# Kernel tuning notes

Hardware: AMD Instinct MI355X
Metric: run time of the kernel (lower is better)

## Reference

```python
import jax, jax.numpy as jnp
import numpy as np
from jax import lax

DIM, D_INNER, D_STATE, D_CONV, DT_RANK = 256, 512, 16, 4, 16
B_, H_, W_ = 4, 64, 64


def setup_inputs() -> dict:
    key = jax.random.key(0)
    ks = jax.random.split(key, 10)
    s = lambda k, shape, scale: (jax.random.normal(k, shape, dtype=jnp.float32) * scale)
    inp = {
        "x": s(ks[0], (B_, DIM, H_, W_), 1.0),
        "in_proj_w": s(ks[1], (2 * D_INNER, DIM), DIM ** -0.5),
        "conv_w": s(ks[2], (D_INNER, 1, D_CONV), D_CONV ** -0.5),
        "conv_b": s(ks[3], (D_INNER,), 0.02),
        "x_proj_w": s(ks[4], (DT_RANK + 2 * D_STATE, D_INNER), D_INNER ** -0.5),
        "dt_proj_w": s(ks[5], (D_INNER, DT_RANK), DT_RANK ** -0.5),
        "dt_proj_b": s(ks[6], (D_INNER,), 0.02),
        # A_log init: log(arange(1..d_state)) broadcast over channels (standard S4D-real init)
        "A_log": jnp.broadcast_to(jnp.log(jnp.arange(1, D_STATE + 1, dtype=jnp.float32)), (D_INNER, D_STATE)).copy(),
        "D": jnp.ones((D_INNER,), dtype=jnp.float32),
        "out_proj_w": s(ks[7], (DIM, D_INNER), D_INNER ** -0.5),
    }
    return inp


def _mamba_forward(x, in_proj_w, conv_w, conv_b, x_proj_w, dt_proj_w, dt_proj_b, A_log, D, out_proj_w):
    b, c, h, w = x.shape
    L = h * w
    xs = x.reshape(b, c, L).transpose(0, 2, 1)                      # [b, L, dim]

    xz = jnp.einsum('bld,ed->ble', xs, in_proj_w)                   # [b, L, 2*d_inner]
    u, res = jnp.split(xz, 2, axis=-1)                              # each [b, L, d_inner]

    # causal depthwise conv1d over sequence
    u_t = u.transpose(0, 2, 1)                                      # [b, d_inner, L]
    u_t = lax.conv_general_dilated(u_t, conv_w, window_strides=(1,),
                                   padding=[(D_CONV - 1, 0)],
                                   feature_group_count=D_INNER,
                                   dimension_numbers=('NCH', 'OIH', 'NCH'))
    u = jax.nn.silu(u_t.transpose(0, 2, 1) + conv_b)                # [b, L, d_inner]

    dbc = jnp.einsum('bld,ed->ble', u, x_proj_w)                    # [b, L, dt_rank+2n]
    dt, Bm, Cm = jnp.split(dbc, [DT_RANK, DT_RANK + D_STATE], axis=-1)
    delta = jax.nn.softplus(jnp.einsum('blr,dr->bld', dt, dt_proj_w) + dt_proj_b)  # [b,L,d_inner]

    A = -jnp.exp(A_log)                                             # [d_inner, n]
    deltaA = jnp.exp(jnp.einsum('bld,dn->bldn', delta, A))          # [b,L,d,n]
    deltaBu = jnp.einsum('bld,bln,bld->bldn', delta, Bm, u)         # [b,L,d,n]

    def step(state, inp):
        dA, dBu, c_t = inp                                          # [b,d,n],[b,d,n],[b,n]
        state = dA * state + dBu
        y = jnp.einsum('bdn,bn->bd', state, c_t)
        return state, y

    init = jnp.zeros((b, D_INNER, D_STATE), dtype=x.dtype)
    _, ys = lax.scan(step, init, (jnp.moveaxis(deltaA, 1, 0),
                                  jnp.moveaxis(deltaBu, 1, 0),
                                  jnp.moveaxis(Cm, 1, 0)))
    y = jnp.moveaxis(ys, 0, 1) + u * D                              # [b, L, d_inner]
    y = y * jax.nn.silu(res)
    out = jnp.einsum('ble,de->bld', y, out_proj_w)                  # [b, L, dim]
    return out.transpose(0, 2, 1).reshape(b, c, h, w)


def reference(x, in_proj_w, conv_w, conv_b, x_proj_w, dt_proj_w, dt_proj_b, A_log, D, out_proj_w):
    return _mamba_forward(x, in_proj_w, conv_w, conv_b, x_proj_w, dt_proj_w, dt_proj_b, A_log, D, out_proj_w)
```

## Files before the change

kernel.cpp:

```cpp
#include <hip/hip_runtime.h>
#include <math.h>


namespace {
constexpr int kB   = 4;
constexpr int kDim = 256;
constexpr int kL   = 4096;
constexpr int kDI  = 512;
constexpr int kN   = 16;
constexpr int kNC  = 128;
constexpr int kCS  = 32;
}

typedef __attribute__((ext_vector_type(8))) short bf16x8;
typedef __attribute__((ext_vector_type(4))) float f32x4;
typedef __attribute__((ext_vector_type(2))) float f32x2;

__device__ __forceinline__ float rcpf(float x) { return __builtin_amdgcn_rcpf(x); }
__device__ __forceinline__ float siluf(float x) { return x * rcpf(1.f + __expf(-x)); }
__device__ __forceinline__ float softplusf(float x) {
  return fmaxf(x, 0.f) + __logf(1.f + __expf(-fabsf(x)));
}

__device__ __forceinline__ unsigned short f2bf(float x) {
  union { float f; unsigned int u; } v; v.f = x;
  unsigned int u = v.u;
  u += 0x7fffu + ((u >> 16) & 1u);
  return (unsigned short)(u >> 16);
}
__device__ __forceinline__ float bf2f(unsigned short u) {
  union { unsigned int i; float f; } v; v.i = ((unsigned int)u) << 16; return v.f;
}

__device__ __forceinline__ void gload_lds16(const void* g, void* l) {
  __builtin_amdgcn_global_load_lds(
      (const __attribute__((address_space(1))) unsigned int*)g,
      (__attribute__((address_space(3))) unsigned int*)l, 16, 0, 0);
}

__global__ __launch_bounds__(256) void k_prep(const float* __restrict__ w_in,
                                              const float* __restrict__ w_out,
                                              const float* __restrict__ w_x,
                                              const float* __restrict__ w_dt,
                                              const float* __restrict__ A_log,
                                              const float* __restrict__ x,
                                              unsigned short* __restrict__ wib,
                                              unsigned short* __restrict__ wob,
                                              unsigned short* __restrict__ wxb,
                                              unsigned short* __restrict__ wdtb,
                                              float* __restrict__ Avz,
                                              unsigned int* __restrict__ flagA,
                                              unsigned short* __restrict__ xt) {
  __shared__ float Xs[64][65];
  const int blk = blockIdx.x;
  const int t = threadIdx.x;
  if (blk < 1760) {
    int idx = blk * 256 + t;
    if (idx < 262144) wib[idx] = f2bf(w_in[idx]);
    else if (idx < 393216) wob[idx - 262144] = f2bf(w_out[idx - 262144]);
    else if (idx < 417792) wxb[idx - 393216] = f2bf(w_x[idx - 393216]);
    else {
      int i = idx - 417792;
      int r = i & 31, d = i >> 5;
      wdtb[i] = (r < 16) ? f2bf(w_dt[d * 16 + r]) : (unsigned short)0;
    }
  } else if (blk < 1762) {
    int d = (blk - 1760) * 256 + t;
    float a0 = -__expf(A_log[d * kN]);
    bool ok = true;
#pragma unroll
    for (int n = 1; n < kN; ++n) {
      float av = -__expf(A_log[d * kN + n]);
      ok = ok && (fabsf(av - (n + 1) * a0) <= 1e-5f * fabsf(av));
    }
    Avz[d] = a0;
    unsigned long long bal = __ballot(ok);
    int wv = t >> 6;
    if ((t & 63) == 0) ((unsigned long long*)Xs)[wv] = bal;
    __syncthreads();
    if (t == 0) {
      unsigned long long all = ~0ull;
#pragma unroll
      for (int w = 0; w < 4; ++w) all &= ((unsigned long long*)Xs)[w];
      flagA[blk - 1760] = (all == ~0ull) ? 1u : 0u;
    }
  } else {
    int id = blk - 1762;
    int lb = id & 63, db = (id >> 6) & 3, b = id >> 8;
    const int d0 = db * 64, l0 = lb * 64, l = t & 63;
#pragma unroll
    for (int rep = 0; rep < 16; ++rep) {
      int dd = rep * 4 + (t >> 6);
      Xs[dd][l] = x[((size_t)b * kDim + d0 + dd) * kL + l0 + l];
    }
    __syncthreads();
#pragma unroll
    for (int rep = 0; rep < 8; ++rep) {
      int lj = rep * 8 + (t >> 5);
      int di = (t & 31) * 2;
      ushort2 v;
      v.x = f2bf(Xs[di][lj]);
      v.y = f2bf(Xs[di + 1][lj]);
      *(ushort2*)(xt + ((size_t)b * kL + l0 + lj) * kDim + d0 + di) = v;
    }
  }
}

__global__ __launch_bounds__(256) void gemm_in_lm(const unsigned short* __restrict__ xt,
                                                  const unsigned short* __restrict__ W,
                                                  unsigned short* __restrict__ ubf,
                                                  unsigned short* __restrict__ resb) {
  __shared__ __align__(16) unsigned short As[128 * 64];
  __shared__ __align__(16) unsigned short Bs[128 * 64];
  const int e0 = blockIdx.x * 128;
  const int l0 = blockIdx.y * 128;
  const int b  = blockIdx.z;
  const int t  = threadIdx.x;
  const int wave = t >> 6, lane = t & 63;
  const int wm = wave >> 1, wn = wave & 1;
  const unsigned short* Ab = xt + (size_t)b * kL * kDim;

  f32x4 acc[4][4];
#pragma unroll
  for (int i = 0; i < 4; ++i)
#pragma unroll
    for (int j = 0; j < 4; ++j) acc[i][j] = (f32x4)0.0f;

  const int srow = t >> 3, sch = t & 7;
  for (int kt = 0; kt < 4; ++kt) {
    const int k0 = kt * 64;
#pragma unroll
    for (int c = 0; c < 4; ++c) {
      int row = c * 32 + srow;
      int gch = sch ^ (row & 7);
      gload_lds16(Ab + (size_t)(l0 + row) * kDim + k0 + gch * 8,
                  (char*)As + c * 4096 + wave * 1024);
      gload_lds16(W  + (size_t)(e0 + row) * kDim + k0 + gch * 8,
                  (char*)Bs + c * 4096 + wave * 1024);
    }
    __syncthreads();
#pragma unroll
    for (int ks = 0; ks < 2; ++ks) {
      bf16x8 af[4], bfr[4];
#pragma unroll
      for (int f = 0; f < 4; ++f) {
        int ra = wm * 64 + f * 16 + (lane & 15);
        int ca = (ks * 4 + (lane >> 4)) ^ (ra & 7);
        af[f] = *(const bf16x8*)((const char*)As + ra * 128 + ca * 16);
        int rb = wn * 64 + f * 16 + (lane & 15);
        int cb = (ks * 4 + (lane >> 4)) ^ (rb & 7);
        bfr[f] = *(const bf16x8*)((const char*)Bs + rb * 128 + cb * 16);
      }
#pragma unroll
      for (int i = 0; i < 4; ++i)
#pragma unroll
        for (int j = 0; j < 4; ++j)
          acc[i][j] = __builtin_amdgcn_mfma_f32_16x16x32_bf16(af[i], bfr[j], acc[i][j], 0, 0, 0);
    }
    __syncthreads();
  }

  const bool is_u = (e0 < kDI);
  unsigned short* dst = is_u ? ubf : resb;
  const int ebase = is_u ? e0 : (e0 - kDI);
#pragma unroll
  for (int i = 0; i < 4; ++i)
#pragma unroll
    for (int j = 0; j < 4; ++j)
#pragma unroll
      for (int r = 0; r < 4; ++r) {
        int l = l0 + wm * 64 + i * 16 + (lane >> 4) * 4 + r;
        int e = ebase + wn * 64 + j * 16 + (lane & 15);
        dst[((size_t)b * kL + l) * kDI + e] = f2bf(acc[i][j][r]);
      }
}

__global__ __launch_bounds__(256) void k_conv(const unsigned short* __restrict__ ubf,
                                              const float* __restrict__ cw,
                                              const float* __restrict__ cb,
                                              unsigned short* __restrict__ ucb) {
  int idx = blockIdx.x * 256 + threadIdx.x;
  int d8 = idx & 63;
  int l  = (idx >> 6) & (kL - 1);
  int b  = idx >> 18;
  int d0 = d8 * 8;
  const unsigned short* row = ubf + ((size_t)b * kL + l) * kDI + d0;
  uint4 zero = make_uint4(0, 0, 0, 0);
  uint4 c0 = *(const uint4*)row;
  uint4 c1 = (l >= 1) ? *(const uint4*)(row - kDI)     : zero;
  uint4 c2 = (l >= 2) ? *(const uint4*)(row - 2 * kDI) : zero;
  uint4 c3 = (l >= 3) ? *(const uint4*)(row - 3 * kDI) : zero;
  const unsigned int* p0 = (const unsigned int*)&c0;
  const unsigned int* p1 = (const unsigned int*)&c1;
  const unsigned int* p2 = (const unsigned int*)&c2;
  const unsigned int* p3 = (const unsigned int*)&c3;
  unsigned short ov[8];
#pragma unroll
  for (int c = 0; c < 8; ++c) {
    int q = c >> 1, hi = c & 1;
    float u0 = bf2f((unsigned short)(hi ? (p0[q] >> 16) : (p0[q] & 0xffff)));
    float u1 = bf2f((unsigned short)(hi ? (p1[q] >> 16) : (p1[q] & 0xffff)));
    float u2 = bf2f((unsigned short)(hi ? (p2[q] >> 16) : (p2[q] & 0xffff)));
    float u3 = bf2f((unsigned short)(hi ? (p3[q] >> 16) : (p3[q] & 0xffff)));
    float4 w = *(const float4*)(cw + (d0 + c) * 4);
    float acc = cb[d0 + c] + w.x * u3 + w.y * u2 + w.z * u1 + w.w * u0;
    ov[c] = f2bf(siluf(acc));
  }
  *(uint4*)(ucb + ((size_t)b * kL + l) * kDI + d0) = *(const uint4*)ov;
}

__global__ __launch_bounds__(256) void k_xproj_dt(const unsigned short* __restrict__ Wx,
                                                  const unsigned short* __restrict__ Wdtb,
                                                  const float* __restrict__ bdt,
                                                  float* __restrict__ dbcBC,
                                                  const unsigned short* __restrict__ ucb,
                                                  unsigned short* __restrict__ delb) {
  __shared__ __align__(16) unsigned short As[64 * 64];
  __shared__ __align__(16) unsigned short Bs[128 * 64];
  __shared__ __align__(16) unsigned short dtTl[128 * 32];
  __shared__ __align__(16) unsigned short Wl[128 * 32];
  const int l0 = blockIdx.x * 128;
  const int b  = blockIdx.y;
  const int t  = threadIdx.x;
  const int wave = t >> 6, lane = t & 63;
  const unsigned short* Bb = ucb + (size_t)b * kL * kDI;

  f32x4 acc[3][2];
#pragma unroll
  for (int i = 0; i < 3; ++i)
#pragma unroll
    for (int j = 0; j < 2; ++j) acc[i][j] = (f32x4)0.0f;

  const int srow = t >> 3, sch = t & 7;
  for (int kt = 0; kt < 8; ++kt) {
    const int k0 = kt * 64;
#pragma unroll
    for (int c = 0; c < 2; ++c) {
      int row = c * 32 + srow;
      int grow = row < 48 ? row : 47;
      int gch = sch ^ (row & 7);
      gload_lds16(Wx + (size_t)grow * kDI + k0 + gch * 8,
                  (char*)As + c * 4096 + wave * 1024);
    }
#pragma unroll
    for (int c = 0; c < 4; ++c) {
      int row = c * 32 + srow;
      int gch = sch ^ (row & 7);
      gload_lds16(Bb + (size_t)(l0 + row) * kDI + k0 + gch * 8,
                  (char*)Bs + c * 4096 + wave * 1024);
    }
    __syncthreads();
#pragma unroll
    for (int ks = 0; ks < 2; ++ks) {
      bf16x8 af[3], bfr[2];
#pragma unroll
      for (int f = 0; f < 3; ++f) {
        int ra = f * 16 + (lane & 15);
        int ca = (ks * 4 + (lane >> 4)) ^ (ra & 7);
        af[f] = *(const bf16x8*)((const char*)As + ra * 128 + ca * 16);
      }
#pragma unroll
      for (int f = 0; f < 2; ++f) {
        int rb = wave * 32 + f * 16 + (lane & 15);
        int cb = (ks * 4 + (lane >> 4)) ^ (rb & 7);
        bfr[f] = *(const bf16x8*)((const char*)Bs + rb * 128 + cb * 16);
      }
#pragma unroll
      for (int i = 0; i < 3; ++i)
#pragma unroll
        for (int j = 0; j < 2; ++j)
          acc[i][j] = __builtin_amdgcn_mfma_f32_16x16x32_bf16(af[i], bfr[j], acc[i][j], 0, 0, 0);
    }
    __syncthreads();
  }

#pragma unroll
  for (int i = 1; i < 3; ++i)
#pragma unroll
    for (int j = 0; j < 2; ++j)
#pragma unroll
      for (int r = 0; r < 4; ++r) {
        int m = i * 16 + (lane >> 4) * 4 + r;
        int l = l0 + wave * 32 + j * 16 + (lane & 15);
        dbcBC[((size_t)b * 32 + (m - 16)) * kL + l] = acc[i][j][r];
      }
#pragma unroll
  for (int j = 0; j < 2; ++j) {
    int l = wave * 32 + j * 16 + (lane & 15);
    int m0 = (lane >> 4) * 4;
    ushort4 v;
    v.x = f2bf(acc[0][j][0]); v.y = f2bf(acc[0][j][1]);
    v.z = f2bf(acc[0][j][2]); v.w = f2bf(acc[0][j][3]);
    int byte = l * 64 + (((m0 >> 3) ^ (l & 3)) << 4) + ((m0 & 7) << 1);
    *(ushort4*)((char*)dtTl + byte) = v;
  }
  {
    int lz = t >> 1, zc = 2 + (t & 1);
    *(uint4*)((char*)dtTl + lz * 64 + ((zc ^ (lz & 3)) << 4)) = make_uint4(0, 0, 0, 0);
  }
  __syncthreads();

  const int wl = wave >> 1, wd = wave & 1;
  for (int dt4 = 0; dt4 < 4; ++dt4) {
#pragma unroll
    for (int c2 = 0; c2 < 2; ++c2) {
      int unit = c2 * 256 + t;
      int row = unit >> 2, sc = unit & 3;
      int gch = sc ^ (row & 3);
      gload_lds16(Wdtb + (size_t)(dt4 * 128 + row) * 32 + gch * 8,
                  (char*)Wl + c2 * 4096 + t * 16);
    }
    __syncthreads();
    f32x4 acc2[4][4];
#pragma unroll
    for (int i = 0; i < 4; ++i)
#pragma unroll
      for (int j = 0; j < 4; ++j) acc2[i][j] = (f32x4)0.0f;
    bf16x8 afr[4], bfr2[4];
#pragma unroll
    for (int f = 0; f < 4; ++f) {
      int ra = wl * 64 + f * 16 + (lane & 15);
      afr[f] = *(const bf16x8*)((const char*)dtTl + ra * 64 + (((lane >> 4) ^ (ra & 3)) << 4));
      int rb = wd * 64 + f * 16 + (lane & 15);
      bfr2[f] = *(const bf16x8*)((const char*)Wl + rb * 64 + (((lane >> 4) ^ (rb & 3)) << 4));
    }
#pragma unroll
    for (int i = 0; i < 4; ++i)
#pragma unroll
      for (int j = 0; j < 4; ++j)
        acc2[i][j] = __builtin_amdgcn_mfma_f32_16x16x32_bf16(afr[i], bfr2[j], acc2[i][j], 0, 0, 0);
#pragma unroll
    for (int j = 0; j < 4; ++j) {
      int d = dt4 * 128 + wd * 64 + j * 16 + (lane & 15);
      float bd = bdt[d];
#pragma unroll
      for (int i = 0; i < 4; ++i)
#pragma unroll
        for (int r = 0; r < 4; ++r) {
          int l = l0 + wl * 64 + i * 16 + (lane >> 4) * 4 + r;
          float delta = softplusf(acc2[i][j][r] + bd);
          delb[((size_t)b * kL + l) * kDI + d] = f2bf(delta);
        }
    }
    __syncthreads();
  }
}

__global__ __launch_bounds__(128) void k_scanA(const unsigned short* __restrict__ delb,
                                               const unsigned short* __restrict__ ucb,
                                               const float* __restrict__ dbcBC,
                                               const float* __restrict__ A_log,
                                               const float* __restrict__ Avz,
                                               const unsigned int* __restrict__ flagA,
                                               float* __restrict__ Pprod,
                                               float* __restrict__ Pfull,
                                               float* __restrict__ S) {
  __shared__ __align__(16) float Bsh[16][kCS];
  const int b = blockIdx.z, ch = blockIdx.y;
  const int t = threadIdx.x;
  const int d = blockIdx.x * 128 + t;
  const int l0 = ch * kCS;
  {
    int row = t >> 3, li = (t & 7) * 4;
    *(float4*)&Bsh[row][li] =
        *(const float4*)&dbcBC[((size_t)b * 32 + row) * kL + l0 + li];
  }
  __syncthreads();
  const bool fast = (flagA[0] != 0u) && (flagA[1] != 0u);
  const float Av0 = Avz[d];
  const unsigned short* pDel = delb + ((size_t)b * kL + l0) * kDI + d;
  const unsigned short* pU = ucb + ((size_t)b * kL + l0) * kDI + d;
  size_t obase = (size_t)(b * kNC + ch) * (kN * kDI) + d;

  if (fast) {
    f32x2 Sv2[8];
#pragma unroll
    for (int m = 0; m < 8; ++m) Sv2[m] = (f32x2){0.f, 0.f};
    float Pp = 1.f;
    for (int i = 0; i < kCS; i += 4) {
      f32x2 a2[4], e2[4], du2[4];
#pragma unroll
      for (int jj = 0; jj < 4; ++jj) {
        float dl = bf2f(pDel[(size_t)(i + jj) * kDI]);
        float uu = bf2f(pU[(size_t)(i + jj) * kDI]);
        float E = __expf(dl * Av0);
        float duv = dl * uu;
        du2[jj] = (f32x2){duv, duv};
        float Esq = E * E;
        a2[jj] = (f32x2){E, Esq};
        e2[jj] = (f32x2){Esq, Esq};
        Pp *= E;
      }
#pragma unroll
      for (int m = 0; m < 8; ++m) {
        float4 Ba = *(const float4*)&Bsh[2 * m][i];
        float4 Bb = *(const float4*)&Bsh[2 * m + 1][i];
        Sv2[m] = Sv2[m] * a2[0] + du2[0] * (f32x2){Ba.x, Bb.x};
        Sv2[m] = Sv2[m] * a2[1] + du2[1] * (f32x2){Ba.y, Bb.y};
        Sv2[m] = Sv2[m] * a2[2] + du2[2] * (f32x2){Ba.z, Bb.z};
        Sv2[m] = Sv2[m] * a2[3] + du2[3] * (f32x2){Ba.w, Bb.w};
        if (m < 7) {
          a2[0] *= e2[0]; a2[1] *= e2[1]; a2[2] *= e2[2]; a2[3] *= e2[3];
        }
      }
    }
    Pprod[(size_t)(b * kNC + ch) * kDI + d] = Pp;
#pragma unroll
    for (int n = 0; n < kN; ++n)
      S[obase + (size_t)n * kDI] = (n & 1) ? Sv2[n >> 1].y : Sv2[n >> 1].x;
  } else {
    float Av[16];
#pragma unroll
    for (int n = 0; n < kN; ++n) Av[n] = -__expf(A_log[d * kN + n]);
    float Pv[16], Sv[16];
#pragma unroll
    for (int n = 0; n < kN; ++n) { Pv[n] = 1.f; Sv[n] = 0.f; }
    for (int i = 0; i < kCS; i += 4) {
      float del[4], du[4];
#pragma unroll
      for (int jj = 0; jj < 4; ++jj) {
        del[jj] = bf2f(pDel[(size_t)(i + jj) * kDI]);
        du[jj] = del[jj] * bf2f(pU[(size_t)(i + jj) * kDI]);
      }
#pragma unroll
      for (int n = 0; n < kN; ++n) {
        float4 B4 = *(const float4*)&Bsh[n][i];
        float a;
        a = __expf(del[0] * Av[n]); Pv[n] *= a; Sv[n] = Sv[n] * a + du[0] * B4.x;
        a = __expf(del[1] * Av[n]); Pv[n] *= a; Sv[n] = Sv[n] * a + du[1] * B4.y;
        a = __expf(del[2] * Av[n]); Pv[n] *= a; Sv[n] = Sv[n] * a + du[2] * B4.z;
        a = __expf(del[3] * Av[n]); Pv[n] *= a; Sv[n] = Sv[n] * a + du[3] * B4.w;
      }
    }
#pragma unroll
    for (int n = 0; n < kN; ++n) {
      Pfull[obase + (size_t)n * kDI] = Pv[n];
      S[obase + (size_t)n * kDI] = Sv[n];
    }
  }
}

__global__ __launch_bounds__(256) void k_scanB(const float* __restrict__ Pprod,
                                               const float* __restrict__ Pfull,
                                               const float* __restrict__ S,
                                               const unsigned int* __restrict__ flagA,
                                               float* __restrict__ init) {
  int idx = blockIdx.x * 256 + threadIdx.x;
  int b = idx >> 13, nd = idx & 8191;
  int n = nd >> 9, d = nd & 511;
  size_t base = (size_t)b * kNC * 8192 + nd;
  const bool fast = (flagA[0] != 0u) && (flagA[1] != 0u);
  float carry = 0.f;
  if (fast) {
    size_t pbase = (size_t)b * kNC * kDI + d;
    const int e = n + 1;
    for (int c0 = 0; c0 < kNC; c0 += 8) {
      float p[8], s[8];
#pragma unroll
      for (int j = 0; j < 8; ++j) {
        float pr = Pprod[pbase + (size_t)(c0 + j) * kDI];
        float p2 = pr * pr, p4 = p2 * p2, p8 = p4 * p4;
        float pw = 1.f;
        if (e & 1) pw *= pr;
        if (e & 2) pw *= p2;
        if (e & 4) pw *= p4;
        if (e & 8) pw *= p8;
        if (e & 16) pw *= p8 * p8;
        p[j] = pw;
        s[j] = S[base + (size_t)(c0 + j) * 8192];
      }
#pragma unroll
      for (int j = 0; j < 8; ++j) {
        init[base + (size_t)(c0 + j) * 8192] = carry;
        carry = p[j] * carry + s[j];
      }
    }
  } else {
    for (int c0 = 0; c0 < kNC; c0 += 8) {
      float p[8], s[8];
#pragma unroll
      for (int j = 0; j < 8; ++j) {
        size_t o = base + (size_t)(c0 + j) * 8192;
        p[j] = Pfull[o]; s[j] = S[o];
      }
#pragma unroll
      for (int j = 0; j < 8; ++j) {
        init[base + (size_t)(c0 + j) * 8192] = carry;
        carry = p[j] * carry + s[j];
      }
    }
  }
}

__global__ __launch_bounds__(128) void k_scanC(const unsigned short* __restrict__ delb,
                                               const unsigned short* __restrict__ ucb,
                                               const float* __restrict__ dbcBC,
                                               const float* __restrict__ A_log,
                                               const float* __restrict__ Avz,
                                               const unsigned int* __restrict__ flagA,
                                               const float* __restrict__ init,
                                               const unsigned short* __restrict__ resb,
                                               const float* __restrict__ Dp,
                                               unsigned short* __restrict__ yt) {
  __shared__ __align__(16) float BCsh[32][kCS];
  const int b = blockIdx.z, ch = blockIdx.y;
  const int t = threadIdx.x;
  const int d = blockIdx.x * 128 + t;
  const int l0 = ch * kCS;
  {
    int row = t >> 2, li = (t & 3) * 8;
    *(float4*)&BCsh[row][li] =
        *(const float4*)&dbcBC[((size_t)b * 32 + row) * kL + l0 + li];
    *(float4*)&BCsh[row][li + 4] =
        *(const float4*)&dbcBC[((size_t)b * 32 + row) * kL + l0 + li + 4];
  }
  __syncthreads();
  const bool fast = (flagA[0] != 0u) && (flagA[1] != 0u);
  const float Av0 = Avz[d];
  const float Dv = Dp[d];
  const unsigned short* pDel = delb + ((size_t)b * kL + l0) * kDI + d;
  const unsigned short* pU = ucb + ((size_t)b * kL + l0) * kDI + d;
  const unsigned short* pR = resb + ((size_t)b * kL + l0) * kDI + d;
  unsigned short* pY = yt + ((size_t)b * kL + l0) * kDI + d;
  size_t ibase = (size_t)(b * kNC + ch) * (kN * kDI) + d;

  if (fast) {
    f32x2 s2[8];
#pragma unroll
    for (int m = 0; m < 8; ++m)
      s2[m] = (f32x2){init[ibase + (size_t)(2 * m) * kDI],
                      init[ibase + (size_t)(2 * m + 1) * kDI]};
    for (int i = 0; i < kCS; i += 4) {
      float uv[4];
      f32x2 a2[4], e2[4], du2[4], yacc2[4];
#pragma unroll
      for (int jj = 0; jj < 4; ++jj) {
        float dl = bf2f(pDel[(size_t)(i + jj) * kDI]);
        uv[jj] = bf2f(pU[(size_t)(i + jj) * kDI]);
        float E = __expf(dl * Av0);
        float duv = dl * uv[jj];
        du2[jj] = (f32x2){duv, duv};
        float Esq = E * E;
        a2[jj] = (f32x2){E, Esq};
        e2[jj] = (f32x2){Esq, Esq};
        yacc2[jj] = (f32x2){0.f, 0.f};
      }
#pragma unroll
      for (int m = 0; m < 8; ++m) {
        float4 Ba = *(const float4*)&BCsh[2 * m][i];
        float4 Bb = *(const float4*)&BCsh[2 * m + 1][i];
        float4 Ca = *(const float4*)&BCsh[16 + 2 * m][i];
        float4 Cb = *(const float4*)&BCsh[16 + 2 * m + 1][i];
        s2[m] = s2[m] * a2[0] + du2[0] * (f32x2){Ba.x, Bb.x};
        yacc2[0] = yacc2[0] + s2[m] * (f32x2){Ca.x, Cb.x};
        s2[m] = s2[m] * a2[1] + du2[1] * (f32x2){Ba.y, Bb.y};
        yacc2[1] = yacc2[1] + s2[m] * (f32x2){Ca.y, Cb.y};
        s2[m] = s2[m] * a2[2] + du2[2] * (f32x2){Ba.z, Bb.z};
        yacc2[2] = yacc2[2] + s2[m] * (f32x2){Ca.z, Cb.z};
        s2[m] = s2[m] * a2[3] + du2[3] * (f32x2){Ba.w, Bb.w};
        yacc2[3] = yacc2[3] + s2[m] * (f32x2){Ca.w, Cb.w};
        if (m < 7) {
          a2[0] *= e2[0]; a2[1] *= e2[1]; a2[2] *= e2[2]; a2[3] *= e2[3];
        }
      }
#pragma unroll
      for (int jj = 0; jj < 4; ++jj) {
        float yv = yacc2[jj].x + yacc2[jj].y;
        float r = bf2f(pR[(size_t)(i + jj) * kDI]);
        float gv = (yv + uv[jj] * Dv) * siluf(r);
        pY[(size_t)(i + jj) * kDI] = f2bf(gv);
      }
    }
  } else {
    float Av[16];
#pragma unroll
    for (int n = 0; n < kN; ++n) Av[n] = -__expf(A_log[d * kN + n]);
    float s[16];
#pragma unroll
    for (int n = 0; n < kN; ++n) s[n] = init[ibase + (size_t)n * kDI];
    for (int i = 0; i < kCS; i += 4) {
      float uv[4], du[4], del[4], yacc[4] = {0.f, 0.f, 0.f, 0.f};
#pragma unroll
      for (int jj = 0; jj < 4; ++jj) {
        del[jj] = bf2f(pDel[(size_t)(i + jj) * kDI]);
        uv[jj] = bf2f(pU[(size_t)(i + jj) * kDI]);
        du[jj] = del[jj] * uv[jj];
      }
#pragma unroll
      for (int n = 0; n < kN; ++n) {
        float4 B4 = *(const float4*)&BCsh[n][i];
        float4 C4 = *(const float4*)&BCsh[16 + n][i];
        float a;
        a = __expf(del[0] * Av[n]); s[n] = s[n] * a + du[0] * B4.x; yacc[0] += s[n] * C4.x;
        a = __expf(del[1] * Av[n]); s[n] = s[n] * a + du[1] * B4.y; yacc[1] += s[n] * C4.y;
        a = __expf(del[2] * Av[n]); s[n] = s[n] * a + du[2] * B4.z; yacc[2] += s[n] * C4.z;
        a = __expf(del[3] * Av[n]); s[n] = s[n] * a + du[3] * B4.w; yacc[3] += s[n] * C4.w;
      }
#pragma unroll
      for (int jj = 0; jj < 4; ++jj) {
        float r = bf2f(pR[(size_t)(i + jj) * kDI]);
        float gv = (yacc[jj] + uv[jj] * Dv) * siluf(r);
        pY[(size_t)(i + jj) * kDI] = f2bf(gv);
      }
    }
  }
}

__global__ __launch_bounds__(256) void gemm_out(const unsigned short* __restrict__ A,
                                                const unsigned short* __restrict__ Bt,
                                                float* __restrict__ C0) {
  __shared__ __align__(16) unsigned short As[128 * 64];
  __shared__ __align__(16) unsigned short Bs[128 * 64];
  const int n0 = blockIdx.x * 128;
  const int m0 = blockIdx.y * 128;
  const int b  = blockIdx.z;
  const int t  = threadIdx.x;
  const int wave = t >> 6, lane = t & 63;
  const int wm = wave >> 1, wn = wave & 1;
  const unsigned short* Bb = Bt + (size_t)b * kL * kDI;

  f32x4 acc[4][4];
#pragma unroll
  for (int i = 0; i < 4; ++i)
#pragma unroll
    for (int j = 0; j < 4; ++j) acc[i][j] = (f32x4)0.0f;

  const int srow = t >> 3, sch = t & 7;
  for (int kt = 0; kt < 8; ++kt) {
    const int k0 = kt * 64;
#pragma unroll
    for (int c = 0; c < 4; ++c) {
      int row = c * 32 + srow;
      int gch = sch ^ (row & 7);
      gload_lds16(A  + (size_t)(m0 + row) * kDI + k0 + gch * 8,
                  (char*)As + c * 4096 + wave * 1024);
      gload_lds16(Bb + (size_t)(n0 + row) * kDI + k0 + gch * 8,
                  (char*)Bs + c * 4096 + wave * 1024);
    }
    __syncthreads();
#pragma unroll
    for (int ks = 0; ks < 2; ++ks) {
      bf16x8 af[4], bfr[4];
#pragma unroll
      for (int f = 0; f < 4; ++f) {
        int ra = wm * 64 + f * 16 + (lane & 15);
        int ca = (ks * 4 + (lane >> 4)) ^ (ra & 7);
        af[f] = *(const bf16x8*)((const char*)As + ra * 128 + ca * 16);
        int rb = wn * 64 + f * 16 + (lane & 15);
        int cb = (ks * 4 + (lane >> 4)) ^ (rb & 7);
        bfr[f] = *(const bf16x8*)((const char*)Bs + rb * 128 + cb * 16);
      }
#pragma unroll
      for (int i = 0; i < 4; ++i)
#pragma unroll
        for (int j = 0; j < 4; ++j)
          acc[i][j] = __builtin_amdgcn_mfma_f32_16x16x32_bf16(af[i], bfr[j], acc[i][j], 0, 0, 0);
    }
    __syncthreads();
  }
#pragma unroll
  for (int i = 0; i < 4; ++i)
#pragma unroll
    for (int j = 0; j < 4; ++j)
#pragma unroll
      for (int r = 0; r < 4; ++r) {
        int m = m0 + wm * 64 + i * 16 + (lane >> 4) * 4 + r;
        int n = n0 + wn * 64 + j * 16 + (lane & 15);
        C0[((size_t)b * kDim + m) * kL + n] = acc[i][j][r];
      }
}

extern "C" void kernel_launch(void* const* d_in, const int* in_sizes, int n_in,
                              void* d_out, int out_size, void* d_ws, size_t ws_size,
                              hipStream_t stream) {
  const float* x       = (const float*)d_in[0];
  const float* in_w    = (const float*)d_in[1];
  const float* conv_w  = (const float*)d_in[2];
  const float* conv_b  = (const float*)d_in[3];
  const float* xproj_w = (const float*)d_in[4];
  const float* dt_w    = (const float*)d_in[5];
  const float* dt_b    = (const float*)d_in[6];
  const float* A_log   = (const float*)d_in[7];
  const float* Dp      = (const float*)d_in[8];
  const float* out_w   = (const float*)d_in[9];
  float* out = (float*)d_out;

  float* ws = (float*)d_ws;
  const size_t nBLD  = (size_t)kB * kL * kDI;
  const size_t nPS   = (size_t)kB * kNC * kN * kDI;
  float* dbcBC  = ws;
  float* Sb     = dbcBC + 524288;
  float* initb  = Sb + nPS;
  float* Pprodb = initb + nPS;
  unsigned short* ubf  = (unsigned short*)(Pprodb + 262144);
  unsigned short* ucb  = ubf + nBLD;
  unsigned short* resb = ucb + nBLD;
  unsigned short* delb = resb + nBLD;
  unsigned short* wib  = delb + nBLD;
  unsigned short* wob  = wib + 262144;
  unsigned short* wxb  = wob + 131072;
  unsigned short* wdtb = wxb + 24576;
  float* Avz           = (float*)(wdtb + 32768);
  unsigned int* flagA  = (unsigned int*)(Avz + 512);
  unsigned short* xt   = delb;
  float* Pfull         = (float*)ubf;
  unsigned short* yt   = (unsigned short*)Sb;

  k_prep<<<dim3(2786), 256, 0, stream>>>(in_w, out_w, xproj_w, dt_w, A_log, x,
                                         wib, wob, wxb, wdtb, Avz, flagA, xt);
  gemm_in_lm<<<dim3(8, kL / 128, kB), 256, 0, stream>>>(xt, wib, ubf, resb);
  k_conv<<<dim3((unsigned)(kB * kL * 64 / 256)), 256, 0, stream>>>(ubf, conv_w, conv_b, ucb);
  k_xproj_dt<<<dim3(kL / 128, kB), 256, 0, stream>>>(wxb, wdtb, dt_b, dbcBC, ucb, delb);
  k_scanA<<<dim3(4, kNC, kB), 128, 0, stream>>>(delb, ucb, dbcBC, A_log, Avz, flagA, Pprodb, Pfull, Sb);
  k_scanB<<<dim3(kB * kDI * kN / 256), 256, 0, stream>>>(Pprodb, Pfull, Sb, flagA, initb);
  k_scanC<<<dim3(4, kNC, kB), 128, 0, stream>>>(delb, ucb, dbcBC, A_log, Avz, flagA, initb, resb, Dp, yt);
  gemm_out<<<dim3(kL / 128, kDim / 128, kB), 256, 0, stream>>>(wob, yt, out);
}
```

Baseline: 156.3 us.

## Rebalance scan chunking, halve x_proj tile, shrink scanB blocks

Doubles the scan chunk length (fewer chunks), which halves the chunk-state buffers and the sequential inter-chunk pass. The x_proj/dt kernel tile shrinks from 128 to 64 sequence positions so twice as many blocks launch, and scanB uses 64-thread blocks for more blocks. Workspace aliasing is reshuffled (yt now overlaps ubf). Longer chunks add serial work per scanA/scanC block but cut their block count.

```diff
diff --git a/kernel.cpp b/kernel.cpp
--- a/kernel.cpp
+++ b/kernel.cpp
@@ -8,8 +8,8 @@
 constexpr int kL   = 4096;
 constexpr int kDI  = 512;
 constexpr int kN   = 16;
-constexpr int kNC  = 128;
-constexpr int kCS  = 32;
+constexpr int kNC  = 64;
+constexpr int kCS  = 64;
 }
 
 typedef __attribute__((ext_vector_type(8))) short bf16x8;
@@ -216,20 +216,18 @@
                                                   const unsigned short* __restrict__ ucb,
                                                   unsigned short* __restrict__ delb) {
   __shared__ __align__(16) unsigned short As[64 * 64];
-  __shared__ __align__(16) unsigned short Bs[128 * 64];
-  __shared__ __align__(16) unsigned short dtTl[128 * 32];
+  __shared__ __align__(16) unsigned short Bs[64 * 64];
+  __shared__ __align__(16) unsigned short dtTl[64 * 32];
   __shared__ __align__(16) unsigned short Wl[128 * 32];
-  const int l0 = blockIdx.x * 128;
+  const int l0 = blockIdx.x * 64;
   const int b  = blockIdx.y;
   const int t  = threadIdx.x;
   const int wave = t >> 6, lane = t & 63;
   const unsigned short* Bb = ucb + (size_t)b * kL * kDI;
 
-  f32x4 acc[3][2];
-#pragma unroll
-  for (int i = 0; i < 3; ++i)
-#pragma unroll
-    for (int j = 0; j < 2; ++j) acc[i][j] = (f32x4)0.0f;
+  f32x4 acc[3];
+#pragma unroll
+  for (int i = 0; i < 3; ++i) acc[i] = (f32x4)0.0f;
 
   const int srow = t >> 3, sch = t & 7;
   for (int kt = 0; kt < 8; ++kt) {
@@ -243,7 +241,7 @@
                   (char*)As + c * 4096 + wave * 1024);
     }
 #pragma unroll
-    for (int c = 0; c < 4; ++c) {
+    for (int c = 0; c < 2; ++c) {
       int row = c * 32 + srow;
       int gch = sch ^ (row & 7);
       gload_lds16(Bb + (size_t)(l0 + row) * kDI + k0 + gch * 8,
@@ -252,24 +250,19 @@
     __syncthreads();
 #pragma unroll
     for (int ks = 0; ks < 2; ++ks) {
-      bf16x8 af[3], bfr[2];
+      bf16x8 af[3], bfr;
 #pragma unroll
       for (int f = 0; f < 3; ++f) {
         int ra = f * 16 + (lane & 15);
         int ca = (ks * 4 + (lane >> 4)) ^ (ra & 7);
         af[f] = *(const bf16x8*)((const char*)As + ra * 128 + ca * 16);
       }
-#pragma unroll
-      for (int f = 0; f < 2; ++f) {
-        int rb = wave * 32 + f * 16 + (lane & 15);
-        int cb = (ks * 4 + (lane >> 4)) ^ (rb & 7);
-        bfr[f] = *(const bf16x8*)((const char*)Bs + rb * 128 + cb * 16);
-      }
+      int rb = wave * 16 + (lane & 15);
+      int cb = (ks * 4 + (lane >> 4)) ^ (rb & 7);
+      bfr = *(const bf16x8*)((const char*)Bs + rb * 128 + cb * 16);
 #pragma unroll
       for (int i = 0; i < 3; ++i)
-#pragma unroll
-        for (int j = 0; j < 2; ++j)
-          acc[i][j] = __builtin_amdgcn_mfma_f32_16x16x32_bf16(af[i], bfr[j], acc[i][j], 0, 0, 0);
+        acc[i] = __builtin_amdgcn_mfma_f32_16x16x32_bf16(af[i], bfr, acc[i], 0, 0, 0);
     }
     __syncthreads();
   }
@@ -277,30 +270,26 @@
 #pragma unroll
   for (int i = 1; i < 3; ++i)
 #pragma unroll
-    for (int j = 0; j < 2; ++j)
-#pragma unroll
-      for (int r = 0; r < 4; ++r) {
-        int m = i * 16 + (lane >> 4) * 4 + r;
-        int l = l0 + wave * 32 + j * 16 + (lane & 15);
-        dbcBC[((size_t)b * 32 + (m - 16)) * kL + l] = acc[i][j][r];
-      }
-#pragma unroll
-  for (int j = 0; j < 2; ++j) {
-    int l = wave * 32 + j * 16 + (lane & 15);
+    for (int r = 0; r < 4; ++r) {
+      int m = i * 16 + (lane >> 4) * 4 + r;
+      int l = l0 + wave * 16 + (lane & 15);
+      dbcBC[((size_t)b * 32 + (m - 16)) * kL + l] = acc[i][r];
+    }
+  {
+    int lloc = wave * 16 + (lane & 15);
     int m0 = (lane >> 4) * 4;
     ushort4 v;
-    v.x = f2bf(acc[0][j][0]); v.y = f2bf(acc[0][j][1]);
-    v.z = f2bf(acc[0][j][2]); v.w = f2bf(acc[0][j][3]);
-    int byte = l * 64 + (((m0 >> 3) ^ (l & 3)) << 4) + ((m0 & 7) << 1);
+    v.x = f2bf(acc[0][0]); v.y = f2bf(acc[0][1]);
+    v.z = f2bf(acc[0][2]); v.w = f2bf(acc[0][3]);
+    int byte = lloc * 64 + (((m0 >> 3) ^ (lloc & 3)) << 4) + ((m0 & 7) << 1);
     *(ushort4*)((char*)dtTl + byte) = v;
   }
-  {
+  if (t < 128) {
     int lz = t >> 1, zc = 2 + (t & 1);
     *(uint4*)((char*)dtTl + lz * 64 + ((zc ^ (lz & 3)) << 4)) = make_uint4(0, 0, 0, 0);
   }
   __syncthreads();
 
-  const int wl = wave >> 1, wd = wave & 1;
   for (int dt4 = 0; dt4 < 4; ++dt4) {
 #pragma unroll
     for (int c2 = 0; c2 < 2; ++c2) {
@@ -311,33 +300,36 @@
                   (char*)Wl + c2 * 4096 + t * 16);
     }
     __syncthreads();
-    f32x4 acc2[4][4];
+    f32x4 acc2[4][2];
 #pragma unroll
     for (int i = 0; i < 4; ++i)
 #pragma unroll
-      for (int j = 0; j < 4; ++j) acc2[i][j] = (f32x4)0.0f;
-    bf16x8 afr[4], bfr2[4];
+      for (int j = 0; j < 2; ++j) acc2[i][j] = (f32x4)0.0f;
+    bf16x8 afr[4], bfr2[2];
 #pragma unroll
     for (int f = 0; f < 4; ++f) {
-      int ra = wl * 64 + f * 16 + (lane & 15);
+      int ra = f * 16 + (lane & 15);
       afr[f] = *(const bf16x8*)((const char*)dtTl + ra * 64 + (((lane >> 4) ^ (ra & 3)) << 4));
-      int rb = wd * 64 + f * 16 + (lane & 15);
+    }
+#pragma unroll
+    for (int f = 0; f < 2; ++f) {
+      int rb = wave * 32 + f * 16 + (lane & 15);
       bfr2[f] = *(const bf16x8*)((const char*)Wl + rb * 64 + (((lane >> 4) ^ (rb & 3)) << 4));
     }
 #pragma unroll
     for (int i = 0; i < 4; ++i)
 #pragma unroll
-      for (int j = 0; j < 4; ++j)
+      for (int j = 0; j < 2; ++j)
         acc2[i][j] = __builtin_amdgcn_mfma_f32_16x16x32_bf16(afr[i], bfr2[j], acc2[i][j], 0, 0, 0);
 #pragma unroll
-    for (int j = 0; j < 4; ++j) {
-      int d = dt4 * 128 + wd * 64 + j * 16 + (lane & 15);
+    for (int j = 0; j < 2; ++j) {
+      int d = dt4 * 128 + wave * 32 + j * 16 + (lane & 15);
       float bd = bdt[d];
 #pragma unroll
       for (int i = 0; i < 4; ++i)
 #pragma unroll
         for (int r = 0; r < 4; ++r) {
-          int l = l0 + wl * 64 + i * 16 + (lane >> 4) * 4 + r;
+          int l = l0 + i * 16 + (lane >> 4) * 4 + r;
           float delta = softplusf(acc2[i][j][r] + bd);
           delb[((size_t)b * kL + l) * kDI + d] = f2bf(delta);
         }
@@ -361,9 +353,11 @@
   const int d = blockIdx.x * 128 + t;
   const int l0 = ch * kCS;
   {
-    int row = t >> 3, li = (t & 7) * 4;
+    int row = t >> 3, li = (t & 7) * 8;
     *(float4*)&Bsh[row][li] =
         *(const float4*)&dbcBC[((size_t)b * 32 + row) * kL + l0 + li];
+    *(float4*)&Bsh[row][li + 4] =
+        *(const float4*)&dbcBC[((size_t)b * 32 + row) * kL + l0 + li + 4];
   }
   __syncthreads();
   const bool fast = (flagA[0] != 0u) && (flagA[1] != 0u);
@@ -440,12 +434,12 @@
   }
 }
 
-__global__ __launch_bounds__(256) void k_scanB(const float* __restrict__ Pprod,
-                                               const float* __restrict__ Pfull,
-                                               const float* __restrict__ S,
-                                               const unsigned int* __restrict__ flagA,
-                                               float* __restrict__ init) {
-  int idx = blockIdx.x * 256 + threadIdx.x;
+__global__ __launch_bounds__(64) void k_scanB(const float* __restrict__ Pprod,
+                                              const float* __restrict__ Pfull,
+                                              const float* __restrict__ S,
+                                              const unsigned int* __restrict__ flagA,
+                                              float* __restrict__ init) {
+  int idx = blockIdx.x * 64 + threadIdx.x;
   int b = idx >> 13, nd = idx & 8191;
   int n = nd >> 9, d = nd & 511;
   size_t base = (size_t)b * kNC * 8192 + nd;
@@ -508,11 +502,11 @@
   const int d = blockIdx.x * 128 + t;
   const int l0 = ch * kCS;
   {
-    int row = t >> 2, li = (t & 3) * 8;
-    *(float4*)&BCsh[row][li] =
-        *(const float4*)&dbcBC[((size_t)b * 32 + row) * kL + l0 + li];
-    *(float4*)&BCsh[row][li + 4] =
-        *(const float4*)&dbcBC[((size_t)b * 32 + row) * kL + l0 + li + 4];
+    int row = t >> 2, li = (t & 3) * 16;
+#pragma unroll
+    for (int q = 0; q < 4; ++q)
+      *(float4*)&BCsh[row][li + q * 4] =
+          *(const float4*)&dbcBC[((size_t)b * 32 + row) * kL + l0 + li + q * 4];
   }
   __syncthreads();
   const bool fast = (flagA[0] != 0u) && (flagA[1] != 0u);
@@ -692,7 +686,7 @@
   float* Sb     = dbcBC + 524288;
   float* initb  = Sb + nPS;
   float* Pprodb = initb + nPS;
-  unsigned short* ubf  = (unsigned short*)(Pprodb + 262144);
+  unsigned short* ubf  = (unsigned short*)(Pprodb + 131072);
   unsigned short* ucb  = ubf + nBLD;
   unsigned short* resb = ucb + nBLD;
   unsigned short* delb = resb + nBLD;
@@ -704,15 +698,15 @@
   unsigned int* flagA  = (unsigned int*)(Avz + 512);
   unsigned short* xt   = delb;
   float* Pfull         = (float*)ubf;
-  unsigned short* yt   = (unsigned short*)Sb;
+  unsigned short* yt   = (unsigned short*)ubf;
 
   k_prep<<<dim3(2786), 256, 0, stream>>>(in_w, out_w, xproj_w, dt_w, A_log, x,
                                          wib, wob, wxb, wdtb, Avz, flagA, xt);
   gemm_in_lm<<<dim3(8, kL / 128, kB), 256, 0, stream>>>(xt, wib, ubf, resb);
   k_conv<<<dim3((unsigned)(kB * kL * 64 / 256)), 256, 0, stream>>>(ubf, conv_w, conv_b, ucb);
-  k_xproj_dt<<<dim3(kL / 128, kB), 256, 0, stream>>>(wxb, wdtb, dt_b, dbcBC, ucb, delb);
+  k_xproj_dt<<<dim3(kL / 64, kB), 256, 0, stream>>>(wxb, wdtb, dt_b, dbcBC, ucb, delb);
   k_scanA<<<dim3(4, kNC, kB), 128, 0, stream>>>(delb, ucb, dbcBC, A_log, Avz, flagA, Pprodb, Pfull, Sb);
-  k_scanB<<<dim3(kB * kDI * kN / 256), 256, 0, stream>>>(Pprodb, Pfull, Sb, flagA, initb);
+  k_scanB<<<dim3(kB * kDI * kN / 64), 64, 0, stream>>>(Pprodb, Pfull, Sb, flagA, initb);
   k_scanC<<<dim3(4, kNC, kB), 128, 0, stream>>>(delb, ucb, dbcBC, A_log, Avz, flagA, initb, resb, Dp, yt);
   gemm_out<<<dim3(kL / 128, kDim / 128, kB), 256, 0, stream>>>(wob, yt, out);
 }
```

After: 141.6 us. -9.4%, faster.
